# Kernel optimization log

Hardware: AMD Instinct MI355X
Metric: run time of the kernel (lower is better)

Reference implementation:

```python
import jax, jax.numpy as jnp
import numpy as np

N_HEADS = 16
HIDDEN = 256
DIM = 4096
SEQ_LEN = 4096
BATCH = 8192
DECAY_CONSTANT = SEQ_LEN // 512  # = 8


def setup_inputs() -> dict:
    key = jax.random.key(0)
    ks = jax.random.split(key, 9)
    return {
        "x": jax.random.normal(ks[0], (BATCH, DIM), dtype=jnp.float32),
        "proj_w": jax.random.normal(ks[1], (N_HEADS, HIDDEN, DIM), dtype=jnp.float32) * 0.02,
        "proj_b": jax.random.normal(ks[2], (N_HEADS, HIDDEN), dtype=jnp.float32) * 0.02,
        "mix_w": jax.random.normal(ks[3], (N_HEADS, SEQ_LEN), dtype=jnp.float32) * 0.02 + 1.0,
        "mix_b": jax.random.normal(ks[4], (N_HEADS, SEQ_LEN), dtype=jnp.float32) * 0.02,
        "decay_value": jax.random.uniform(ks[5], (N_HEADS,), dtype=jnp.float32, minval=0.85, maxval=1.05),
        "cache": jax.random.normal(ks[6], (N_HEADS, BATCH, HIDDEN), dtype=jnp.float32),
        "out_w": jax.random.normal(ks[7], (DIM, DIM), dtype=jnp.float32) * 0.02,
        "out_b": jax.random.normal(ks[8], (DIM,), dtype=jnp.float32) * 0.02,
        "index": 1000,
    }


def reference(x, proj_w, proj_b, mix_w, mix_b, decay_value, cache, out_w, out_b, index):
    # Per-head projections: [h, b, k]
    proj = jnp.einsum("bd,hkd->hbk", x, proj_w) + proj_b[:, None, :]

    # Mixer params at the given sequence index (scalar per head)
    w = mix_w[:, index]          # [h]
    b = mix_b[:, index]          # [h]
    decay = jnp.clip(decay_value, 0.9, 1.0) ** (1.0 / DECAY_CONSTANT)  # [h]

    # First n_heads//2 heads are Col-style: out = w*x + w*decay*cache + b
    # Last  n_heads//2 heads are Row-style: out = w*x +   decay*cache + b
    is_col = jnp.arange(N_HEADS) < (N_HEADS // 2)
    cache_coef = jnp.where(is_col, w * decay, decay)  # [h]

    out = (w[:, None, None] * proj
           + cache_coef[:, None, None] * cache
           + b[:, None, None])  # [h, b, k]

    # Concatenate heads along feature axis -> [batch, n_heads*hidden] = [batch, dim]
    hidden = jnp.transpose(out, (1, 0, 2)).reshape(x.shape[0], N_HEADS * HIDDEN)

    return hidden @ out_w.T + out_b
```

## Files before the change

kernel.cpp:

```cpp
#include <hip/hip_runtime.h>
#include <hip/hip_bf16.h>

#define MROW 8192
#define DIMK 4096
#define NCOL 4096
#define HID  256
#define NH   16
#define SEQL 4096

#define BKT 32
#define NKT (DIMK / BKT)
#define SLOTB 32768
#define LDS_TOTAL (4 * SLOTB)
#define NGEMM ((MROW / 256) * (NCOL / 256))
#define NCVT 256

typedef __attribute__((ext_vector_type(8))) short short8;
typedef __attribute__((ext_vector_type(4))) float f32x4;

__device__ inline ushort f2bf(float f) {
  unsigned u = __float_as_uint(f);
  u += 0x7FFF + ((u >> 16) & 1);
  return (ushort)(u >> 16);
}

__device__ inline void gload16(const void* g, void* l) {
  __builtin_amdgcn_global_load_lds(
      (const __attribute__((address_space(1))) void*)g,
      (__attribute__((address_space(3))) void*)l, 16, 0, 0);
}

__device__ inline void cvt8(const float* __restrict__ s, ushort* __restrict__ d, long i) {
  const float4* s4 = (const float4*)(s + i * 8);
  float4 a = s4[0], b = s4[1];
  ushort r[8] = {f2bf(a.x), f2bf(a.y), f2bf(a.z), f2bf(a.w),
                 f2bf(b.x), f2bf(b.y), f2bf(b.z), f2bf(b.w)};
  *(uint4*)(d + i * 8) = *(const uint4*)r;
}

__global__ void cvt_xpw(const float* __restrict__ x, ushort* __restrict__ xb,
                        const float* __restrict__ pw, ushort* __restrict__ pwb) {
  const long n8x = (long)MROW * DIMK / 8;
  const long n8p = (long)NCOL * DIMK / 8;
  long stride = (long)gridDim.x * blockDim.x;
  for (long i = (long)blockIdx.x * blockDim.x + threadIdx.x; i < n8x + n8p; i += stride) {
    if (i < n8x) cvt8(x, xb, i);
    else         cvt8(pw, pwb, i - n8x);
  }
}

__global__ void coef_kernel(const float* __restrict__ mix_w, const float* __restrict__ mix_b,
                            const float* __restrict__ decay_value, const float* __restrict__ proj_b,
                            const int* __restrict__ index_p,
                            float* __restrict__ wv, float* __restrict__ cc, float* __restrict__ pb2) {
  int n = blockIdx.x * blockDim.x + threadIdx.x;
  if (n >= NCOL) return;
  int h = n >> 8;
  int idx = *index_p;
  float w  = mix_w[h * SEQL + idx];
  float bb = mix_b[h * SEQL + idx];
  float dv = fminf(fmaxf(decay_value[h], 0.9f), 1.0f);
  float decay = powf(dv, 0.125f);
  float coef = (h < NH / 2) ? w * decay : decay;
  wv[n]  = w;
  cc[n]  = coef;
  pb2[n] = w * proj_b[n] + bb;
}

template <int EPI>
__global__ __launch_bounds__(1024, 4) void gemm256(
    const ushort* __restrict__ A, const ushort* __restrict__ B,
    float* __restrict__ outf, ushort* __restrict__ outh,
    const float* __restrict__ cache, const float* __restrict__ wv,
    const float* __restrict__ cc, const float* __restrict__ pb2,
    const float* __restrict__ outb,
    const float* __restrict__ owsrc, ushort* __restrict__ owdst) {
  extern __shared__ __align__(16) char smem[];

  const int bid = blockIdx.x;
  if (EPI == 1 && bid >= NGEMM) {
    const long n8 = (long)NCOL * DIMK / 8;
    long stride = (long)NCVT * blockDim.x;
    for (long i = (long)(bid - NGEMM) * blockDim.x + threadIdx.x; i < n8; i += stride)
      cvt8(owsrc, owdst, i);
    return;
  }

  const int tid  = threadIdx.x;
  const int lane = tid & 63;
  const int wid  = tid >> 6;
  const int wr = wid >> 2;
  const int wc = wid & 3;
  const int r16 = lane & 15;
  const int cq  = lane >> 4;

  const int swz = (bid & 7) * 64 + (bid >> 3);
  const int bm = swz >> 4, bn = swz & 15;
  const int m0 = bm * 256, n0 = bn * 256;

  const ushort* Ag = A + (size_t)m0 * DIMK;
  const ushort* Bg = B + (size_t)n0 * DIMK;

  int aoff[4], boff[4];
#pragma unroll
  for (int i = 0; i < 4; ++i) {
    int arow = wr * 64 + i * 16 + r16;
    aoff[i] = arow * 64 + ((cq ^ ((arow >> 1) & 3)) << 4);
    int brow = wc * 64 + i * 16 + r16;
    boff[i] = 16384 + brow * 64 + ((cq ^ ((brow >> 1) & 3)) << 4);
  }

  const int soff = tid * 16;
  const int srow = soff >> 6;
  const int sgo  = srow * DIMK + ((((soff >> 4) & 3) ^ ((srow >> 1) & 3)) << 3);

  f32x4 acc[4][4] = {};

#pragma unroll
  for (int kt = 0; kt < 3; ++kt) {
    char* s = smem + kt * SLOTB;
    gload16(Ag + (size_t)sgo + kt * BKT, s + soff);
    gload16(Bg + (size_t)sgo + kt * BKT, s + 16384 + soff);
  }
  asm volatile("s_waitcnt vmcnt(4)" ::: "memory");
  __builtin_amdgcn_s_barrier();
  __builtin_amdgcn_sched_barrier(0);

  for (int kt = 0; kt < NKT; ++kt) {
    const char* cur = smem + (kt & 3) * SLOTB;

    short8 af[4], bf[4];
#pragma unroll
    for (int i = 0; i < 4; ++i) bf[i] = *(const short8*)(cur + boff[i]);
#pragma unroll
    for (int i = 0; i < 4; ++i) af[i] = *(const short8*)(cur + aoff[i]);

    if (kt < NKT - 3) {
      char* st = smem + ((kt + 3) & 3) * SLOTB;
      int k0 = (kt + 3) * BKT;
      gload16(Ag + (size_t)sgo + k0, st + soff);
      gload16(Bg + (size_t)sgo + k0, st + 16384 + soff);
    }

    __builtin_amdgcn_s_setprio(1);
#pragma unroll
    for (int mi = 0; mi < 4; ++mi)
#pragma unroll
      for (int ni = 0; ni < 4; ++ni)
        acc[mi][ni] = __builtin_amdgcn_mfma_f32_16x16x32_bf16(af[mi], bf[ni], acc[mi][ni], 0, 0, 0);
    __builtin_amdgcn_s_setprio(0);

    if (kt < NKT - 3)       asm volatile("s_waitcnt vmcnt(4)" ::: "memory");
    else if (kt == NKT - 3) asm volatile("s_waitcnt vmcnt(2)" ::: "memory");
    else if (kt == NKT - 2) asm volatile("s_waitcnt vmcnt(0)" ::: "memory");
    __builtin_amdgcn_s_barrier();
    __builtin_amdgcn_sched_barrier(0);
  }

  const int colb = n0 + wc * 64 + r16;
  const int rowb = m0 + wr * 64 + cq * 4;

  float wvv[4], ccv[4], pbv[4], obv[4];
#pragma unroll
  for (int ni = 0; ni < 4; ++ni) {
    int n = colb + ni * 16;
    if (EPI == 1) { wvv[ni] = wv[n]; ccv[ni] = cc[n]; pbv[ni] = pb2[n]; }
    else          { obv[ni] = outb[n]; }
  }

#pragma unroll
  for (int mi = 0; mi < 4; ++mi) {
#pragma unroll
    for (int ni = 0; ni < 4; ++ni) {
      f32x4 v = acc[mi][ni];
      int n = colb + ni * 16;
#pragma unroll
      for (int r = 0; r < 4; ++r) {
        int m = rowb + mi * 16 + r;
        if (EPI == 1) {
          int h = n >> 8, kq = n & 255;
          float val = wvv[ni] * v[r] + ccv[ni] * cache[((size_t)h * MROW + m) * HID + kq] + pbv[ni];
          outh[(size_t)m * NCOL + n] = f2bf(val);
        } else {
          outf[(size_t)m * NCOL + n] = v[r] + obv[ni];
        }
      }
    }
  }
}

extern "C" void kernel_launch(void* const* d_in, const int* in_sizes, int n_in,
                              void* d_out, int out_size, void* d_ws, size_t ws_size,
                              hipStream_t stream) {
  const float* x      = (const float*)d_in[0];
  const float* proj_w = (const float*)d_in[1];
  const float* proj_b = (const float*)d_in[2];
  const float* mix_w  = (const float*)d_in[3];
  const float* mix_b  = (const float*)d_in[4];
  const float* decay  = (const float*)d_in[5];
  const float* cache  = (const float*)d_in[6];
  const float* out_w  = (const float*)d_in[7];
  const float* out_b  = (const float*)d_in[8];
  const int*   index  = (const int*)d_in[9];

  char* ws = (char*)d_ws;
  ushort* xb  = (ushort*)ws;
  ushort* pwb = (ushort*)(ws + 67108864);
  ushort* owb = (ushort*)(ws + 100663296);
  ushort* hid = (ushort*)(ws + 134217728);
  float*  wv  = (float*)(ws + 201326592);
  float*  cc  = (float*)(ws + 201326592 + 16384);
  float*  pb2 = (float*)(ws + 201326592 + 32768);

  hipFuncSetAttribute((const void*)&gemm256<1>, hipFuncAttributeMaxDynamicSharedMemorySize, LDS_TOTAL);
  hipFuncSetAttribute((const void*)&gemm256<0>, hipFuncAttributeMaxDynamicSharedMemorySize, LDS_TOTAL);

  hipLaunchKernelGGL(cvt_xpw, dim3(3072), dim3(256), 0, stream, x, xb, proj_w, pwb);
  hipLaunchKernelGGL(coef_kernel, dim3(16), dim3(256), 0, stream,
                     mix_w, mix_b, decay, proj_b, index, wv, cc, pb2);

  hipLaunchKernelGGL((gemm256<1>), dim3(NGEMM + NCVT), dim3(1024), LDS_TOTAL, stream,
                     xb, pwb, nullptr, hid, cache, wv, cc, pb2, nullptr, out_w, owb);
  hipLaunchKernelGGL((gemm256<0>), dim3(NGEMM), dim3(1024), LDS_TOTAL, stream,
                     hid, owb, (float*)d_out, nullptr, nullptr, nullptr, nullptr, nullptr, out_b,
                     nullptr, nullptr);
}
```

Before: 586.6 us.

## Shrink GEMM tiles to 128x128 with 3-stage static LDS pipeline, fuse coef kernel

Replaces the 256x256 tile, 1024-thread GEMM that used a 4-slot, 128KB dynamic LDS ring with a 128x128 tile, 256-thread GEMM that uses a 3-slot, 48KB static LDS ring. The goal is more resident blocks per CU and better load balance across CUs. The coefficient kernel now runs as extra blocks of the conversion kernel, which saves one launch. In exchange, the smaller tiles read A and B from global memory more times per output and pipeline only two stages ahead.

Measured after the change: 830.1 us. 41.5% more time.

```diff
diff --git a/kernel.cpp b/kernel.cpp
--- a/kernel.cpp
+++ b/kernel.cpp
@@ -10,9 +10,8 @@
 
 #define BKT 32
 #define NKT (DIMK / BKT)
-#define SLOTB 32768
-#define LDS_TOTAL (4 * SLOTB)
-#define NGEMM ((MROW / 256) * (NCOL / 256))
+#define SLOTB 16384
+#define NGEMM ((MROW / 128) * (NCOL / 128))
 #define NCVT 256
 
 typedef __attribute__((ext_vector_type(8))) short short8;
@@ -39,43 +38,45 @@
 }
 
 __global__ void cvt_xpw(const float* __restrict__ x, ushort* __restrict__ xb,
-                        const float* __restrict__ pw, ushort* __restrict__ pwb) {
+                        const float* __restrict__ pw, ushort* __restrict__ pwb,
+                        const float* __restrict__ mix_w, const float* __restrict__ mix_b,
+                        const float* __restrict__ decay_value, const float* __restrict__ proj_b,
+                        const int* __restrict__ index_p,
+                        float* __restrict__ wv, float* __restrict__ cc, float* __restrict__ pb2) {
+  const int CVB = 3056;
+  if (blockIdx.x >= CVB) {
+    int n = (blockIdx.x - CVB) * 256 + threadIdx.x;
+    if (n < NCOL) {
+      int h = n >> 8;
+      int idx = *index_p;
+      float w  = mix_w[h * SEQL + idx];
+      float bb = mix_b[h * SEQL + idx];
+      float dv = fminf(fmaxf(decay_value[h], 0.9f), 1.0f);
+      float decay = powf(dv, 0.125f);
+      wv[n]  = w;
+      cc[n]  = (h < NH / 2) ? w * decay : decay;
+      pb2[n] = w * proj_b[n] + bb;
+    }
+    return;
+  }
   const long n8x = (long)MROW * DIMK / 8;
   const long n8p = (long)NCOL * DIMK / 8;
-  long stride = (long)gridDim.x * blockDim.x;
+  long stride = (long)CVB * blockDim.x;
   for (long i = (long)blockIdx.x * blockDim.x + threadIdx.x; i < n8x + n8p; i += stride) {
     if (i < n8x) cvt8(x, xb, i);
     else         cvt8(pw, pwb, i - n8x);
   }
 }
 
-__global__ void coef_kernel(const float* __restrict__ mix_w, const float* __restrict__ mix_b,
-                            const float* __restrict__ decay_value, const float* __restrict__ proj_b,
-                            const int* __restrict__ index_p,
-                            float* __restrict__ wv, float* __restrict__ cc, float* __restrict__ pb2) {
-  int n = blockIdx.x * blockDim.x + threadIdx.x;
-  if (n >= NCOL) return;
-  int h = n >> 8;
-  int idx = *index_p;
-  float w  = mix_w[h * SEQL + idx];
-  float bb = mix_b[h * SEQL + idx];
-  float dv = fminf(fmaxf(decay_value[h], 0.9f), 1.0f);
-  float decay = powf(dv, 0.125f);
-  float coef = (h < NH / 2) ? w * decay : decay;
-  wv[n]  = w;
-  cc[n]  = coef;
-  pb2[n] = w * proj_b[n] + bb;
-}
-
 template <int EPI>
-__global__ __launch_bounds__(1024, 4) void gemm256(
+__global__ __launch_bounds__(256, 3) void gemm128(
     const ushort* __restrict__ A, const ushort* __restrict__ B,
     float* __restrict__ outf, ushort* __restrict__ outh,
     const float* __restrict__ cache, const float* __restrict__ wv,
     const float* __restrict__ cc, const float* __restrict__ pb2,
     const float* __restrict__ outb,
     const float* __restrict__ owsrc, ushort* __restrict__ owdst) {
-  extern __shared__ __align__(16) char smem[];
+  __shared__ __align__(16) char smem[3 * SLOTB];
 
   const int bid = blockIdx.x;
   if (EPI == 1 && bid >= NGEMM) {
@@ -89,14 +90,14 @@
   const int tid  = threadIdx.x;
   const int lane = tid & 63;
   const int wid  = tid >> 6;
-  const int wr = wid >> 2;
-  const int wc = wid & 3;
+  const int wr = wid >> 1;
+  const int wc = wid & 1;
   const int r16 = lane & 15;
   const int cq  = lane >> 4;
 
-  const int swz = (bid & 7) * 64 + (bid >> 3);
-  const int bm = swz >> 4, bn = swz & 15;
-  const int m0 = bm * 256, n0 = bn * 256;
+  const int swz = (bid & 7) * 256 + (bid >> 3);
+  const int bm = swz >> 5, bn = swz & 31;
+  const int m0 = bm * 128, n0 = bn * 128;
 
   const ushort* Ag = A + (size_t)m0 * DIMK;
   const ushort* Bg = B + (size_t)n0 * DIMK;
@@ -107,27 +108,36 @@
     int arow = wr * 64 + i * 16 + r16;
     aoff[i] = arow * 64 + ((cq ^ ((arow >> 1) & 3)) << 4);
     int brow = wc * 64 + i * 16 + r16;
-    boff[i] = 16384 + brow * 64 + ((cq ^ ((brow >> 1) & 3)) << 4);
-  }
-
-  const int soff = tid * 16;
-  const int srow = soff >> 6;
-  const int sgo  = srow * DIMK + ((((soff >> 4) & 3) ^ ((srow >> 1) & 3)) << 3);
+    boff[i] = 8192 + brow * 64 + ((cq ^ ((brow >> 1) & 3)) << 4);
+  }
+
+  int soff[2], sgo[2];
+#pragma unroll
+  for (int j = 0; j < 2; ++j) {
+    int off = j * 4096 + tid * 16;
+    int row = off >> 6;
+    soff[j] = off;
+    sgo[j]  = row * DIMK + ((((off >> 4) & 3) ^ ((row >> 1) & 3)) << 3);
+  }
 
   f32x4 acc[4][4] = {};
 
 #pragma unroll
-  for (int kt = 0; kt < 3; ++kt) {
+  for (int kt = 0; kt < 2; ++kt) {
     char* s = smem + kt * SLOTB;
-    gload16(Ag + (size_t)sgo + kt * BKT, s + soff);
-    gload16(Bg + (size_t)sgo + kt * BKT, s + 16384 + soff);
+#pragma unroll
+    for (int j = 0; j < 2; ++j) {
+      gload16(Ag + (size_t)sgo[j] + kt * BKT, s + soff[j]);
+      gload16(Bg + (size_t)sgo[j] + kt * BKT, s + 8192 + soff[j]);
+    }
   }
   asm volatile("s_waitcnt vmcnt(4)" ::: "memory");
   __builtin_amdgcn_s_barrier();
   __builtin_amdgcn_sched_barrier(0);
 
+  int rcur = 0, rstg = 2;
   for (int kt = 0; kt < NKT; ++kt) {
-    const char* cur = smem + (kt & 3) * SLOTB;
+    const char* cur = smem + rcur * SLOTB;
 
     short8 af[4], bf[4];
 #pragma unroll
@@ -135,11 +145,14 @@
 #pragma unroll
     for (int i = 0; i < 4; ++i) af[i] = *(const short8*)(cur + aoff[i]);
 
-    if (kt < NKT - 3) {
-      char* st = smem + ((kt + 3) & 3) * SLOTB;
-      int k0 = (kt + 3) * BKT;
-      gload16(Ag + (size_t)sgo + k0, st + soff);
-      gload16(Bg + (size_t)sgo + k0, st + 16384 + soff);
+    if (kt < NKT - 2) {
+      char* st = smem + rstg * SLOTB;
+      int k0 = (kt + 2) * BKT;
+#pragma unroll
+      for (int j = 0; j < 2; ++j) {
+        gload16(Ag + (size_t)sgo[j] + k0, st + soff[j]);
+        gload16(Bg + (size_t)sgo[j] + k0, st + 8192 + soff[j]);
+      }
     }
 
     __builtin_amdgcn_s_setprio(1);
@@ -150,11 +163,13 @@
         acc[mi][ni] = __builtin_amdgcn_mfma_f32_16x16x32_bf16(af[mi], bf[ni], acc[mi][ni], 0, 0, 0);
     __builtin_amdgcn_s_setprio(0);
 
-    if (kt < NKT - 3)       asm volatile("s_waitcnt vmcnt(4)" ::: "memory");
-    else if (kt == NKT - 3) asm volatile("s_waitcnt vmcnt(2)" ::: "memory");
+    if (kt < NKT - 2)       asm volatile("s_waitcnt vmcnt(4)" ::: "memory");
     else if (kt == NKT - 2) asm volatile("s_waitcnt vmcnt(0)" ::: "memory");
     __builtin_amdgcn_s_barrier();
     __builtin_amdgcn_sched_barrier(0);
+
+    rcur = (rcur == 2) ? 0 : rcur + 1;
+    rstg = (rstg == 2) ? 0 : rstg + 1;
   }
 
   const int colb = n0 + wc * 64 + r16;
@@ -212,16 +227,13 @@
   float*  cc  = (float*)(ws + 201326592 + 16384);
   float*  pb2 = (float*)(ws + 201326592 + 32768);
 
-  hipFuncSetAttribute((const void*)&gemm256<1>, hipFuncAttributeMaxDynamicSharedMemorySize, LDS_TOTAL);
-  hipFuncSetAttribute((const void*)&gemm256<0>, hipFuncAttributeMaxDynamicSharedMemorySize, LDS_TOTAL);
-
-  hipLaunchKernelGGL(cvt_xpw, dim3(3072), dim3(256), 0, stream, x, xb, proj_w, pwb);
-  hipLaunchKernelGGL(coef_kernel, dim3(16), dim3(256), 0, stream,
+  hipLaunchKernelGGL(cvt_xpw, dim3(3072), dim3(256), 0, stream,
+                     x, xb, proj_w, pwb,
                      mix_w, mix_b, decay, proj_b, index, wv, cc, pb2);
 
-  hipLaunchKernelGGL((gemm256<1>), dim3(NGEMM + NCVT), dim3(1024), LDS_TOTAL, stream,
+  hipLaunchKernelGGL((gemm128<1>), dim3(NGEMM + NCVT), dim3(256), 0, stream,
                      xb, pwb, nullptr, hid, cache, wv, cc, pb2, nullptr, out_w, owb);
-  hipLaunchKernelGGL((gemm256<0>), dim3(NGEMM), dim3(1024), LDS_TOTAL, stream,
+  hipLaunchKernelGGL((gemm128<0>), dim3(NGEMM), dim3(256), 0, stream,
                      hid, owb, (float*)d_out, nullptr, nullptr, nullptr, nullptr, nullptr, out_b,
                      nullptr, nullptr);
 }
```

## Unroll GEMM main loop by two with one barrier per pair; fold coef kernel into convert

Applied to the files above, without the earlier changes.

The bf16 GEMM main loop now handles two K-tiles per iteration. It prefetches two tiles ahead instead of three, and drains all outstanding loads with a single barrier per pair instead of per tile. The goal is to halve barrier and wait overhead in the K loop. The cost is a shorter prefetch distance and a full vmcnt(0) wait, which may expose more global-load latency. Separately, the small coefficient kernel is merged into the conversion kernel as extra trailing blocks, removing one kernel launch.

Measured after the change: 618.6 us. 1.05x slower.

```diff
diff --git a/kernel.cpp b/kernel.cpp
--- a/kernel.cpp
+++ b/kernel.cpp
@@ -39,32 +39,34 @@
 }
 
 __global__ void cvt_xpw(const float* __restrict__ x, ushort* __restrict__ xb,
-                        const float* __restrict__ pw, ushort* __restrict__ pwb) {
+                        const float* __restrict__ pw, ushort* __restrict__ pwb,
+                        const float* __restrict__ mix_w, const float* __restrict__ mix_b,
+                        const float* __restrict__ decay_value, const float* __restrict__ proj_b,
+                        const int* __restrict__ index_p,
+                        float* __restrict__ wv, float* __restrict__ cc, float* __restrict__ pb2) {
+  const int CVB = 3056;
+  if (blockIdx.x >= CVB) {
+    int n = (blockIdx.x - CVB) * 256 + threadIdx.x;
+    if (n < NCOL) {
+      int h = n >> 8;
+      int idx = *index_p;
+      float w  = mix_w[h * SEQL + idx];
+      float bb = mix_b[h * SEQL + idx];
+      float dv = fminf(fmaxf(decay_value[h], 0.9f), 1.0f);
+      float decay = powf(dv, 0.125f);
+      wv[n]  = w;
+      cc[n]  = (h < NH / 2) ? w * decay : decay;
+      pb2[n] = w * proj_b[n] + bb;
+    }
+    return;
+  }
   const long n8x = (long)MROW * DIMK / 8;
   const long n8p = (long)NCOL * DIMK / 8;
-  long stride = (long)gridDim.x * blockDim.x;
+  long stride = (long)CVB * blockDim.x;
   for (long i = (long)blockIdx.x * blockDim.x + threadIdx.x; i < n8x + n8p; i += stride) {
     if (i < n8x) cvt8(x, xb, i);
     else         cvt8(pw, pwb, i - n8x);
   }
-}
-
-__global__ void coef_kernel(const float* __restrict__ mix_w, const float* __restrict__ mix_b,
-                            const float* __restrict__ decay_value, const float* __restrict__ proj_b,
-                            const int* __restrict__ index_p,
-                            float* __restrict__ wv, float* __restrict__ cc, float* __restrict__ pb2) {
-  int n = blockIdx.x * blockDim.x + threadIdx.x;
-  if (n >= NCOL) return;
-  int h = n >> 8;
-  int idx = *index_p;
-  float w  = mix_w[h * SEQL + idx];
-  float bb = mix_b[h * SEQL + idx];
-  float dv = fminf(fmaxf(decay_value[h], 0.9f), 1.0f);
-  float decay = powf(dv, 0.125f);
-  float coef = (h < NH / 2) ? w * decay : decay;
-  wv[n]  = w;
-  cc[n]  = coef;
-  pb2[n] = w * proj_b[n] + bb;
 }
 
 template <int EPI>
@@ -117,42 +119,60 @@
   f32x4 acc[4][4] = {};
 
 #pragma unroll
-  for (int kt = 0; kt < 3; ++kt) {
+  for (int kt = 0; kt < 2; ++kt) {
     char* s = smem + kt * SLOTB;
     gload16(Ag + (size_t)sgo + kt * BKT, s + soff);
     gload16(Bg + (size_t)sgo + kt * BKT, s + 16384 + soff);
   }
-  asm volatile("s_waitcnt vmcnt(4)" ::: "memory");
+  asm volatile("s_waitcnt vmcnt(0)" ::: "memory");
   __builtin_amdgcn_s_barrier();
   __builtin_amdgcn_sched_barrier(0);
 
-  for (int kt = 0; kt < NKT; ++kt) {
-    const char* cur = smem + (kt & 3) * SLOTB;
-
-    short8 af[4], bf[4];
-#pragma unroll
-    for (int i = 0; i < 4; ++i) bf[i] = *(const short8*)(cur + boff[i]);
-#pragma unroll
-    for (int i = 0; i < 4; ++i) af[i] = *(const short8*)(cur + aoff[i]);
-
-    if (kt < NKT - 3) {
-      char* st = smem + ((kt + 3) & 3) * SLOTB;
-      int k0 = (kt + 3) * BKT;
-      gload16(Ag + (size_t)sgo + k0, st + soff);
-      gload16(Bg + (size_t)sgo + k0, st + 16384 + soff);
-    }
-
-    __builtin_amdgcn_s_setprio(1);
-#pragma unroll
-    for (int mi = 0; mi < 4; ++mi)
-#pragma unroll
-      for (int ni = 0; ni < 4; ++ni)
-        acc[mi][ni] = __builtin_amdgcn_mfma_f32_16x16x32_bf16(af[mi], bf[ni], acc[mi][ni], 0, 0, 0);
-    __builtin_amdgcn_s_setprio(0);
-
-    if (kt < NKT - 3)       asm volatile("s_waitcnt vmcnt(4)" ::: "memory");
-    else if (kt == NKT - 3) asm volatile("s_waitcnt vmcnt(2)" ::: "memory");
-    else if (kt == NKT - 2) asm volatile("s_waitcnt vmcnt(0)" ::: "memory");
+  for (int j2 = 0; j2 < NKT; j2 += 2) {
+    {
+      const char* cur = smem + (j2 & 3) * SLOTB;
+      short8 af[4], bf[4];
+#pragma unroll
+      for (int i = 0; i < 4; ++i) bf[i] = *(const short8*)(cur + boff[i]);
+#pragma unroll
+      for (int i = 0; i < 4; ++i) af[i] = *(const short8*)(cur + aoff[i]);
+      if (j2 + 2 < NKT) {
+        char* st = smem + ((j2 + 2) & 3) * SLOTB;
+        int k0 = (j2 + 2) * BKT;
+        gload16(Ag + (size_t)sgo + k0, st + soff);
+        gload16(Bg + (size_t)sgo + k0, st + 16384 + soff);
+      }
+      __builtin_amdgcn_s_setprio(1);
+#pragma unroll
+      for (int mi = 0; mi < 4; ++mi)
+#pragma unroll
+        for (int ni = 0; ni < 4; ++ni)
+          acc[mi][ni] = __builtin_amdgcn_mfma_f32_16x16x32_bf16(af[mi], bf[ni], acc[mi][ni], 0, 0, 0);
+      __builtin_amdgcn_s_setprio(0);
+    }
+    {
+      const char* cur = smem + ((j2 + 1) & 3) * SLOTB;
+      short8 af[4], bf[4];
+#pragma unroll
+      for (int i = 0; i < 4; ++i) bf[i] = *(const short8*)(cur + boff[i]);
+#pragma unroll
+      for (int i = 0; i < 4; ++i) af[i] = *(const short8*)(cur + aoff[i]);
+      if (j2 + 3 < NKT) {
+        char* st = smem + ((j2 + 3) & 3) * SLOTB;
+        int k0 = (j2 + 3) * BKT;
+        gload16(Ag + (size_t)sgo + k0, st + soff);
+        gload16(Bg + (size_t)sgo + k0, st + 16384 + soff);
+      }
+      __builtin_amdgcn_s_setprio(1);
+#pragma unroll
+      for (int mi = 0; mi < 4; ++mi)
+#pragma unroll
+        for (int ni = 0; ni < 4; ++ni)
+          acc[mi][ni] = __builtin_amdgcn_mfma_f32_16x16x32_bf16(af[mi], bf[ni], acc[mi][ni], 0, 0, 0);
+      __builtin_amdgcn_s_setprio(0);
+    }
+
+    asm volatile("s_waitcnt vmcnt(0)" ::: "memory");
     __builtin_amdgcn_s_barrier();
     __builtin_amdgcn_sched_barrier(0);
   }
@@ -215,8 +235,8 @@
   hipFuncSetAttribute((const void*)&gemm256<1>, hipFuncAttributeMaxDynamicSharedMemorySize, LDS_TOTAL);
   hipFuncSetAttribute((const void*)&gemm256<0>, hipFuncAttributeMaxDynamicSharedMemorySize, LDS_TOTAL);
 
-  hipLaunchKernelGGL(cvt_xpw, dim3(3072), dim3(256), 0, stream, x, xb, proj_w, pwb);
-  hipLaunchKernelGGL(coef_kernel, dim3(16), dim3(256), 0, stream,
+  hipLaunchKernelGGL(cvt_xpw, dim3(3072), dim3(256), 0, stream,
+                     x, xb, proj_w, pwb,
                      mix_w, mix_b, decay, proj_b, index, wv, cc, pb2);
 
   hipLaunchKernelGGL((gemm256<1>), dim3(NGEMM + NCVT), dim3(1024), LDS_TOTAL, stream,
```
